# Optimization experiments

Measured on AMD Instinct MI355X. Metric: run time of the kernel, lower is better.

## Reference

```python
import jax, jax.numpy as jnp
import numpy as np

N = 8192
IN_F = 256
OUT_F = 64
ALPHA = 0.3  # LeakyReLU negative slope
NEG_INF = -9e15


def setup_inputs() -> dict:
    key = jax.random.key(0)
    k1, k2, k3, k4 = jax.random.split(key, 4)
    h = jax.random.normal(k1, (N, IN_F), dtype=jnp.float32)
    # sparse-ish binary adjacency with self loops (values are 0/1 floats)
    adj = (jax.random.uniform(k2, (N, N)) < 0.05).astype(jnp.float32)
    adj = jnp.maximum(adj, jnp.eye(N, dtype=jnp.float32))
    # xavier_uniform-style scales (gain=1.414)
    w_lim = 1.414 * np.sqrt(6.0 / (IN_F + OUT_F))
    a_lim = 1.414 * np.sqrt(6.0 / (2 * OUT_F + 1))
    W = jax.random.uniform(k3, (IN_F, OUT_F), minval=-w_lim, maxval=w_lim, dtype=jnp.float32)
    a = jax.random.uniform(k4, (2 * OUT_F, 1), minval=-a_lim, maxval=a_lim, dtype=jnp.float32)
    return {"h": h, "adj": adj, "W": W, "a": a}


def reference(h, adj, W, a):
    # Wh: [N, F]
    Wh = h @ W
    # Additive decomposition of the original concat-attention:
    # e_ij = leakyrelu(a[:F].Wh_i + a[F:].Wh_j)  -- identical math, no NxNx2F tensor
    src = Wh @ a[:OUT_F]      # [N, 1]
    dst = Wh @ a[OUT_F:]      # [N, 1]
    e = jax.nn.leaky_relu(src + dst.T, negative_slope=ALPHA)  # [N, N]
    e = e * adj               # faithful: original multiplies by adj before masking
    att = jnp.where(adj > 0, e, NEG_INF)
    att = jax.nn.softmax(att, axis=1)
    # dropout omitted (eval mode / deterministic reference)
    h_prime = att @ Wh        # [N, F]
    return jax.nn.elu(h_prime)
```

## Files before the change

### kernel.cpp

```cpp
#include <hip/hip_runtime.h>
#include <hip/hip_bf16.h>

#define N_NODES 8192
#define IN_F    256
#define OUT_F   64
#define ALPHA   0.3f
#define MBIAS   20.0f
#define CSPL    8
#define COLS_PER (N_NODES / CSPL)
#define NTILES  (COLS_PER / 64)
#define ROWS    32
#define LDP     72
#define MROW    136

typedef unsigned short u16;
typedef unsigned int   u32;
typedef unsigned long long u64;
typedef __attribute__((ext_vector_type(8))) short bf16x8;
typedef __attribute__((ext_vector_type(4))) float f32x4;

__device__ __forceinline__ float bf2f(u32 u) { return __uint_as_float(u << 16); }
__device__ __forceinline__ u32 f2bfbits(float x) {
    u32 u = __float_as_uint(x);
    return (u + 0x7FFFu + ((u >> 16) & 1u)) >> 16;
}
__device__ __forceinline__ float lrelu(float s) { return s > 0.f ? s : ALPHA * s; }

__device__ __forceinline__ int detect_bf16(const void* adj) {
    return ((((const u32*)adj)[0] & 0xFFFFu) == 0x3F80u) ? 1 : 0;
}

template <bool BF16>
__device__ __forceinline__ float ld(const void* p, size_t idx) {
    if constexpr (BF16) return bf2f(((const u16*)p)[idx]);
    else                return ((const float*)p)[idx];
}

__global__ __launch_bounds__(256) void gat_mask_kernel(
    const void* __restrict__ adj, u64* __restrict__ mask64)
{
    const int lane = threadIdx.x & 63;
    const int wgid = blockIdx.x * 4 + (threadIdx.x >> 6);
    const int NW   = 2048 * 4;
    const int C    = (N_NODES / 256) * N_NODES;

    if (detect_bf16(adj)) {
        const u16* base = (const u16*)adj;
        for (int c = wgid; c < C; c += NW) {
            const u16* p = base + (size_t)c * 256;
            u64 b0 = __ballot(p[lane]       != 0);
            u64 b1 = __ballot(p[64  + lane] != 0);
            u64 b2 = __ballot(p[128 + lane] != 0);
            u64 b3 = __ballot(p[192 + lane] != 0);
            u64 v = (lane == 0) ? b0 : (lane == 1) ? b1 : (lane == 2) ? b2 : b3;
            if (lane < 4) mask64[(size_t)c * 4 + lane] = v;
        }
    } else {
        const float* base = (const float*)adj;
        for (int c = wgid; c < C; c += NW) {
            const float* p = base + (size_t)c * 256;
            u64 b0 = __ballot(p[lane]       != 0.f);
            u64 b1 = __ballot(p[64  + lane] != 0.f);
            u64 b2 = __ballot(p[128 + lane] != 0.f);
            u64 b3 = __ballot(p[192 + lane] != 0.f);
            u64 v = (lane == 0) ? b0 : (lane == 1) ? b1 : (lane == 2) ? b2 : b3;
            if (lane < 4) mask64[(size_t)c * 4 + lane] = v;
        }
    }
}

template <bool BF16>
__device__ __forceinline__ void wh4_impl(
    const void* __restrict__ h, const void* __restrict__ W,
    const void* __restrict__ a, float* __restrict__ src,
    float* __restrict__ dst, int i0, int lane, float* accv)
{
    float acc0 = 0.f, acc1 = 0.f, acc2 = 0.f, acc3 = 0.f;
#pragma unroll 8
    for (int k = 0; k < IN_F; ++k) {
        float wv = ld<BF16>(W, (size_t)k * OUT_F + lane);
        float h0 = ld<BF16>(h, (size_t)(i0 + 0) * IN_F + k);
        float h1 = ld<BF16>(h, (size_t)(i0 + 1) * IN_F + k);
        float h2 = ld<BF16>(h, (size_t)(i0 + 2) * IN_F + k);
        float h3 = ld<BF16>(h, (size_t)(i0 + 3) * IN_F + k);
        acc0 = fmaf(h0, wv, acc0);
        acc1 = fmaf(h1, wv, acc1);
        acc2 = fmaf(h2, wv, acc2);
        acc3 = fmaf(h3, wv, acc3);
    }
    float av = ld<BF16>(a, lane);
    float bv = ld<BF16>(a, OUT_F + lane);
    float accs[4] = {acc0, acc1, acc2, acc3};
#pragma unroll
    for (int r = 0; r < 4; ++r) {
        float ps = accs[r] * av, pd = accs[r] * bv;
#pragma unroll
        for (int off = 32; off > 0; off >>= 1) {
            ps += __shfl_xor(ps, off, 64);
            pd += __shfl_xor(pd, off, 64);
        }
        if (lane == 0) { src[i0 + r] = ps; dst[i0 + r] = pd; }
        accv[r] = accs[r];
    }
}

__global__ __launch_bounds__(256) void gat_wh_kernel(
    const void* __restrict__ h, const void* __restrict__ W,
    const void* __restrict__ a, const void* __restrict__ adj,
    u16* __restrict__ WhT, float* __restrict__ src, float* __restrict__ dst)
{
    __shared__ float accs[16][OUT_F];
    const int tid = threadIdx.x, wave = tid >> 6, lane = tid & 63;
    const int i0 = blockIdx.x * 16 + wave * 4;
    float av[4];
    if (detect_bf16(adj)) wh4_impl<true >(h, W, a, src, dst, i0, lane, av);
    else                  wh4_impl<false>(h, W, a, src, dst, i0, lane, av);
#pragma unroll
    for (int r = 0; r < 4; ++r) accs[wave * 4 + r][lane] = av[r];
    __syncthreads();
    if (tid < OUT_F) {
        u32 w[8];
#pragma unroll
        for (int e = 0; e < 8; ++e) {
            u32 lo = f2bfbits(accs[2 * e][tid]);
            u32 hi = f2bfbits(accs[2 * e + 1][tid]);
            w[e] = lo | (hi << 16);
        }
        u16* dstp = WhT + (size_t)tid * N_NODES + blockIdx.x * 16;
        *(uint4*)dstp       = *(uint4*)&w[0];
        *(uint4*)(dstp + 8) = *(uint4*)&w[4];
    }
}

__global__ __launch_bounds__(256, 4) void gat_attn_kernel(
    const u64* __restrict__ mask64, const u16* __restrict__ WhT,
    const float* __restrict__ src, const float* __restrict__ dst,
    float* __restrict__ O_part, float* __restrict__ l_part)
{
    __shared__ alignas(16) u16 Plds[ROWS * LDP];
    __shared__ alignas(16) u16 Blds[64 * LDP];
    __shared__ alignas(16) unsigned char Mlds[ROWS * MROW];

    const int tid = threadIdx.x, wave = tid >> 6, lane = tid & 63;
    const int r  = tid >> 3, cq = tid & 7;
    const int br = tid >> 2, bq = tid & 3;
    const int i0 = blockIdx.x * ROWS, c0 = blockIdx.y * COLS_PER;

    {
        const unsigned char* mb = (const unsigned char*)mask64;
        uint4 v = *(const uint4*)(mb + (size_t)(i0 + (tid >> 3)) * (N_NODES / 8)
                                     + (c0 >> 3) + (tid & 7) * 16);
        *(uint4*)&Mlds[(tid >> 3) * MROW + (tid & 7) * 16] = v;
    }

    const float srow = src[i0 + r];
    const float m = lrelu(srow + MBIAS);

    const u16*    whtrow = WhT + (size_t)br * N_NODES + c0 + bq * 16;
    const float4* dstp   = (const float4*)(dst + c0 + cq * 8);

    const int mw = wave & 1, nw = wave >> 1;
    const int mrow = lane & 15, kq = (lane >> 4) * 8;

    f32x4 acc[2] = {{0,0,0,0},{0,0,0,0}};
    float lacc = 0.f;

    __syncthreads();

    for (int t = 0; t < NTILES; ++t) {
        uint4 b0 = *(const uint4*)(whtrow + t * 64);
        uint4 b1 = *(const uint4*)(whtrow + t * 64 + 8);
        *(uint4*)&Blds[br * LDP + bq * 16]     = b0;
        *(uint4*)&Blds[br * LDP + bq * 16 + 8] = b1;

        u32 msk = Mlds[r * MROW + t * 8 + cq];
        float4 d0 = dstp[t * 16], d1 = dstp[t * 16 + 1];
        float dv[8] = {d0.x,d0.y,d0.z,d0.w, d1.x,d1.y,d1.z,d1.w};
        u32 po[4];
#pragma unroll
        for (int e = 0; e < 4; ++e) {
            float s0 = lrelu(srow + dv[2 * e]);
            float s1 = lrelu(srow + dv[2 * e + 1]);
            float p0 = (msk & (1u << (2 * e)))     ? __expf(s0 - m) : 0.f;
            float p1 = (msk & (1u << (2 * e + 1))) ? __expf(s1 - m) : 0.f;
            u32 q0 = f2bfbits(p0), q1 = f2bfbits(p1);
            lacc += bf2f(q0) + bf2f(q1);
            po[e] = q0 | (q1 << 16);
        }
        *(uint4*)&Plds[r * LDP + cq * 8] = *(uint4*)&po[0];

        __syncthreads();

#pragma unroll
        for (int ks = 0; ks < 2; ++ks) {
            bf16x8 avf = *(bf16x8*)&Plds[(16 * mw + mrow) * LDP + ks * 32 + kq];
#pragma unroll
            for (int nt2 = 0; nt2 < 2; ++nt2) {
                int nt = nw * 2 + nt2;
                bf16x8 bvf = *(bf16x8*)&Blds[(16 * nt + mrow) * LDP + ks * 32 + kq];
                acc[nt2] = __builtin_amdgcn_mfma_f32_16x16x32_bf16(avf, bvf, acc[nt2], 0, 0, 0);
            }
        }
        __syncthreads();
    }

    lacc += __shfl_xor(lacc, 1, 64);
    lacc += __shfl_xor(lacc, 2, 64);
    lacc += __shfl_xor(lacc, 4, 64);
    if (cq == 0) l_part[blockIdx.y * N_NODES + i0 + r] = lacc;

    float* Ob = O_part + (size_t)blockIdx.y * N_NODES * OUT_F;
#pragma unroll
    for (int nt2 = 0; nt2 < 2; ++nt2) {
        int nt = nw * 2 + nt2;
#pragma unroll
        for (int reg = 0; reg < 4; ++reg) {
            int row = i0 + 16 * mw + (lane >> 4) * 4 + reg;
            int col = 16 * nt + (lane & 15);
            Ob[(size_t)row * OUT_F + col] = acc[nt2][reg];
        }
    }
}

__global__ __launch_bounds__(256) void gat_reduce_kernel(
    const float* __restrict__ O_part, const float* __restrict__ l_part,
    const void* __restrict__ adj, void* __restrict__ out)
{
    int gid = blockIdx.x * 256 + threadIdx.x;
    int i = gid >> 6;
    float O = 0.f, L = 0.f;
#pragma unroll
    for (int c = 0; c < CSPL; ++c) {
        O += O_part[(size_t)c * N_NODES * OUT_F + gid];
        L += l_part[c * N_NODES + i];
    }
    float hp = O / L;
    float o = hp > 0.f ? hp : expm1f(hp);
    if (detect_bf16(adj)) ((u16*)out)[gid] = (u16)f2bfbits(o);
    else                  ((float*)out)[gid] = o;
}

extern "C" void kernel_launch(void* const* d_in, const int* in_sizes, int n_in,
                              void* d_out, int out_size, void* d_ws, size_t ws_size,
                              hipStream_t stream)
{
    const void* h   = d_in[0];
    const void* adj = d_in[1];
    const void* W   = d_in[2];
    const void* a   = d_in[3];

    char* ws = (char*)d_ws;
    u16*   WhT    = (u16*)ws;
    float* src    = (float*)(ws + (1u << 20));
    float* dst    = (float*)(ws + (1u << 20) + 32768);
    u64*   mask64 = (u64*)  (ws + (2u << 20));
    float* O_part = (float*)(ws + (16u << 20));
    float* l_part = (float*)(ws + (32u << 20));

    gat_mask_kernel<<<2048, 256, 0, stream>>>(adj, mask64);
    gat_wh_kernel<<<N_NODES / 16, 256, 0, stream>>>(h, W, a, adj, WhT, src, dst);
    dim3 grid(N_NODES / ROWS, CSPL);
    gat_attn_kernel<<<grid, 256, 0, stream>>>(mask64, WhT, src, dst, O_part, l_part);
    gat_reduce_kernel<<<N_NODES * OUT_F / 256, 256, 0, stream>>>(O_part, l_part, adj, d_out);
}
```

Before: 426.8 us.

## Fuse mask and Wh prep kernels, enlarge attention row tile to 64, prefetch WhT

Merges the adjacency-bitmask kernel and the Wh projection kernel into one launch, splitting the two jobs across block ranges so both run concurrently. The attention kernel now processes 64 rows per block instead of 32, with each wave owning 16 rows across all four output column tiles. This halves how often each WhT tile is reloaded and lets every thread build 16 probabilities per tile. The next WhT tile is also prefetched into registers while the MFMAs run. The costs are more registers, fewer blocks in the grid (1024 rather than 2048), and more LDS per block.

```diff
diff --git a/kernel.cpp b/kernel.cpp
--- a/kernel.cpp
+++ b/kernel.cpp
@@ -9,9 +9,9 @@
 #define CSPL    8
 #define COLS_PER (N_NODES / CSPL)
 #define NTILES  (COLS_PER / 64)
-#define ROWS    32
 #define LDP     72
 #define MROW    136
+#define WH_BLOCKS (N_NODES / 16)
 
 typedef unsigned short u16;
 typedef unsigned int   u32;
@@ -34,39 +34,6 @@
 __device__ __forceinline__ float ld(const void* p, size_t idx) {
     if constexpr (BF16) return bf2f(((const u16*)p)[idx]);
     else                return ((const float*)p)[idx];
-}
-
-__global__ __launch_bounds__(256) void gat_mask_kernel(
-    const void* __restrict__ adj, u64* __restrict__ mask64)
-{
-    const int lane = threadIdx.x & 63;
-    const int wgid = blockIdx.x * 4 + (threadIdx.x >> 6);
-    const int NW   = 2048 * 4;
-    const int C    = (N_NODES / 256) * N_NODES;
-
-    if (detect_bf16(adj)) {
-        const u16* base = (const u16*)adj;
-        for (int c = wgid; c < C; c += NW) {
-            const u16* p = base + (size_t)c * 256;
-            u64 b0 = __ballot(p[lane]       != 0);
-            u64 b1 = __ballot(p[64  + lane] != 0);
-            u64 b2 = __ballot(p[128 + lane] != 0);
-            u64 b3 = __ballot(p[192 + lane] != 0);
-            u64 v = (lane == 0) ? b0 : (lane == 1) ? b1 : (lane == 2) ? b2 : b3;
-            if (lane < 4) mask64[(size_t)c * 4 + lane] = v;
-        }
-    } else {
-        const float* base = (const float*)adj;
-        for (int c = wgid; c < C; c += NW) {
-            const float* p = base + (size_t)c * 256;
-            u64 b0 = __ballot(p[lane]       != 0.f);
-            u64 b1 = __ballot(p[64  + lane] != 0.f);
-            u64 b2 = __ballot(p[128 + lane] != 0.f);
-            u64 b3 = __ballot(p[192 + lane] != 0.f);
-            u64 v = (lane == 0) ? b0 : (lane == 1) ? b1 : (lane == 2) ? b2 : b3;
-            if (lane < 4) mask64[(size_t)c * 4 + lane] = v;
-        }
-    }
 }
 
 template <bool BF16>
@@ -104,31 +71,63 @@
     }
 }
 
-__global__ __launch_bounds__(256) void gat_wh_kernel(
+__global__ __launch_bounds__(256) void gat_prep_kernel(
     const void* __restrict__ h, const void* __restrict__ W,
     const void* __restrict__ a, const void* __restrict__ adj,
-    u16* __restrict__ WhT, float* __restrict__ src, float* __restrict__ dst)
+    u16* __restrict__ WhT, float* __restrict__ src, float* __restrict__ dst,
+    u64* __restrict__ mask64)
 {
     __shared__ float accs[16][OUT_F];
     const int tid = threadIdx.x, wave = tid >> 6, lane = tid & 63;
-    const int i0 = blockIdx.x * 16 + wave * 4;
-    float av[4];
-    if (detect_bf16(adj)) wh4_impl<true >(h, W, a, src, dst, i0, lane, av);
-    else                  wh4_impl<false>(h, W, a, src, dst, i0, lane, av);
-#pragma unroll
-    for (int r = 0; r < 4; ++r) accs[wave * 4 + r][lane] = av[r];
-    __syncthreads();
-    if (tid < OUT_F) {
-        u32 w[8];
-#pragma unroll
-        for (int e = 0; e < 8; ++e) {
-            u32 lo = f2bfbits(accs[2 * e][tid]);
-            u32 hi = f2bfbits(accs[2 * e + 1][tid]);
-            w[e] = lo | (hi << 16);
-        }
-        u16* dstp = WhT + (size_t)tid * N_NODES + blockIdx.x * 16;
-        *(uint4*)dstp       = *(uint4*)&w[0];
-        *(uint4*)(dstp + 8) = *(uint4*)&w[4];
+    const int isbf = detect_bf16(adj);
+
+    if (blockIdx.x < WH_BLOCKS) {
+        const int i0 = blockIdx.x * 16 + wave * 4;
+        float av[4];
+        if (isbf) wh4_impl<true >(h, W, a, src, dst, i0, lane, av);
+        else      wh4_impl<false>(h, W, a, src, dst, i0, lane, av);
+#pragma unroll
+        for (int r = 0; r < 4; ++r) accs[wave * 4 + r][lane] = av[r];
+        __syncthreads();
+        if (tid < OUT_F) {
+            u32 w[8];
+#pragma unroll
+            for (int e = 0; e < 8; ++e) {
+                u32 lo = f2bfbits(accs[2 * e][tid]);
+                u32 hi = f2bfbits(accs[2 * e + 1][tid]);
+                w[e] = lo | (hi << 16);
+            }
+            u16* dstp = WhT + (size_t)tid * N_NODES + blockIdx.x * 16;
+            *(uint4*)dstp       = *(uint4*)&w[0];
+            *(uint4*)(dstp + 8) = *(uint4*)&w[4];
+        }
+    } else {
+        const int wgid = (blockIdx.x - WH_BLOCKS) * 4 + wave;
+        const int NW   = 2048 * 4;
+        const int C    = (N_NODES / 256) * N_NODES;
+        if (isbf) {
+            const u16* base = (const u16*)adj;
+            for (int c = wgid; c < C; c += NW) {
+                const u16* p = base + (size_t)c * 256;
+                u64 b0 = __ballot(p[lane]       != 0);
+                u64 b1 = __ballot(p[64  + lane] != 0);
+                u64 b2 = __ballot(p[128 + lane] != 0);
+                u64 b3 = __ballot(p[192 + lane] != 0);
+                u64 v = (lane == 0) ? b0 : (lane == 1) ? b1 : (lane == 2) ? b2 : b3;
+                if (lane < 4) mask64[(size_t)c * 4 + lane] = v;
+            }
+        } else {
+            const float* base = (const float*)adj;
+            for (int c = wgid; c < C; c += NW) {
+                const float* p = base + (size_t)c * 256;
+                u64 b0 = __ballot(p[lane]       != 0.f);
+                u64 b1 = __ballot(p[64  + lane] != 0.f);
+                u64 b2 = __ballot(p[128 + lane] != 0.f);
+                u64 b3 = __ballot(p[192 + lane] != 0.f);
+                u64 v = (lane == 0) ? b0 : (lane == 1) ? b1 : (lane == 2) ? b2 : b3;
+                if (lane < 4) mask64[(size_t)c * 4 + lane] = v;
+            }
+        }
     }
 }
 
@@ -137,48 +136,50 @@
     const float* __restrict__ src, const float* __restrict__ dst,
     float* __restrict__ O_part, float* __restrict__ l_part)
 {
-    __shared__ alignas(16) u16 Plds[ROWS * LDP];
+    __shared__ alignas(16) u16 Plds[64 * LDP];
     __shared__ alignas(16) u16 Blds[64 * LDP];
-    __shared__ alignas(16) unsigned char Mlds[ROWS * MROW];
+    __shared__ alignas(16) unsigned char Mlds[64 * MROW];
 
     const int tid = threadIdx.x, wave = tid >> 6, lane = tid & 63;
-    const int r  = tid >> 3, cq = tid & 7;
-    const int br = tid >> 2, bq = tid & 3;
-    const int i0 = blockIdx.x * ROWS, c0 = blockIdx.y * COLS_PER;
+    const int r = tid >> 2, cq = tid & 3;
+    const int i0 = blockIdx.x * 64, c0 = blockIdx.y * COLS_PER;
 
     {
-        const unsigned char* mb = (const unsigned char*)mask64;
-        uint4 v = *(const uint4*)(mb + (size_t)(i0 + (tid >> 3)) * (N_NODES / 8)
-                                     + (c0 >> 3) + (tid & 7) * 16);
-        *(uint4*)&Mlds[(tid >> 3) * MROW + (tid & 7) * 16] = v;
+        const unsigned char* g = (const unsigned char*)mask64
+            + (size_t)(i0 + r) * (N_NODES / 8) + (c0 >> 3) + cq * 32;
+        *(uint4*)&Mlds[r * MROW + cq * 32]      = *(const uint4*)g;
+        *(uint4*)&Mlds[r * MROW + cq * 32 + 16] = *(const uint4*)(g + 16);
     }
 
     const float srow = src[i0 + r];
     const float m = lrelu(srow + MBIAS);
 
-    const u16*    whtrow = WhT + (size_t)br * N_NODES + c0 + bq * 16;
-    const float4* dstp   = (const float4*)(dst + c0 + cq * 8);
-
-    const int mw = wave & 1, nw = wave >> 1;
+    const u16*    whtrow = WhT + (size_t)r * N_NODES + c0 + cq * 16;
+    const float4* dstp   = (const float4*)(dst + c0 + cq * 16);
+
     const int mrow = lane & 15, kq = (lane >> 4) * 8;
 
-    f32x4 acc[2] = {{0,0,0,0},{0,0,0,0}};
+    f32x4 acc[4] = {{0,0,0,0},{0,0,0,0},{0,0,0,0},{0,0,0,0}};
     float lacc = 0.f;
 
+    uint4 pb0 = *(const uint4*)(whtrow);
+    uint4 pb1 = *(const uint4*)(whtrow + 8);
+
     __syncthreads();
+    const u16* mrowp = (const u16*)&Mlds[r * MROW];
 
     for (int t = 0; t < NTILES; ++t) {
-        uint4 b0 = *(const uint4*)(whtrow + t * 64);
-        uint4 b1 = *(const uint4*)(whtrow + t * 64 + 8);
-        *(uint4*)&Blds[br * LDP + bq * 16]     = b0;
-        *(uint4*)&Blds[br * LDP + bq * 16 + 8] = b1;
-
-        u32 msk = Mlds[r * MROW + t * 8 + cq];
-        float4 d0 = dstp[t * 16], d1 = dstp[t * 16 + 1];
-        float dv[8] = {d0.x,d0.y,d0.z,d0.w, d1.x,d1.y,d1.z,d1.w};
-        u32 po[4];
-#pragma unroll
-        for (int e = 0; e < 4; ++e) {
+        *(uint4*)&Blds[r * LDP + cq * 16]     = pb0;
+        *(uint4*)&Blds[r * LDP + cq * 16 + 8] = pb1;
+
+        u32 msk = mrowp[t * 4 + cq];
+        float4 d0 = dstp[t * 16],     d1 = dstp[t * 16 + 1];
+        float4 d2 = dstp[t * 16 + 2], d3 = dstp[t * 16 + 3];
+        float dv[16] = {d0.x,d0.y,d0.z,d0.w, d1.x,d1.y,d1.z,d1.w,
+                        d2.x,d2.y,d2.z,d2.w, d3.x,d3.y,d3.z,d3.w};
+        u32 po[8];
+#pragma unroll
+        for (int e = 0; e < 8; ++e) {
             float s0 = lrelu(srow + dv[2 * e]);
             float s1 = lrelu(srow + dv[2 * e + 1]);
             float p0 = (msk & (1u << (2 * e)))     ? __expf(s0 - m) : 0.f;
@@ -187,18 +188,23 @@
             lacc += bf2f(q0) + bf2f(q1);
             po[e] = q0 | (q1 << 16);
         }
-        *(uint4*)&Plds[r * LDP + cq * 8] = *(uint4*)&po[0];
+        *(uint4*)&Plds[r * LDP + cq * 16]     = *(uint4*)&po[0];
+        *(uint4*)&Plds[r * LDP + cq * 16 + 8] = *(uint4*)&po[4];
 
         __syncthreads();
 
+        if (t + 1 < NTILES) {
+            pb0 = *(const uint4*)(whtrow + (t + 1) * 64);
+            pb1 = *(const uint4*)(whtrow + (t + 1) * 64 + 8);
+        }
+
 #pragma unroll
         for (int ks = 0; ks < 2; ++ks) {
-            bf16x8 avf = *(bf16x8*)&Plds[(16 * mw + mrow) * LDP + ks * 32 + kq];
-#pragma unroll
-            for (int nt2 = 0; nt2 < 2; ++nt2) {
-                int nt = nw * 2 + nt2;
+            bf16x8 avf = *(bf16x8*)&Plds[(16 * wave + mrow) * LDP + ks * 32 + kq];
+#pragma unroll
+            for (int nt = 0; nt < 4; ++nt) {
                 bf16x8 bvf = *(bf16x8*)&Blds[(16 * nt + mrow) * LDP + ks * 32 + kq];
-                acc[nt2] = __builtin_amdgcn_mfma_f32_16x16x32_bf16(avf, bvf, acc[nt2], 0, 0, 0);
+                acc[nt] = __builtin_amdgcn_mfma_f32_16x16x32_bf16(avf, bvf, acc[nt], 0, 0, 0);
             }
         }
         __syncthreads();
@@ -206,20 +212,17 @@
 
     lacc += __shfl_xor(lacc, 1, 64);
     lacc += __shfl_xor(lacc, 2, 64);
-    lacc += __shfl_xor(lacc, 4, 64);
     if (cq == 0) l_part[blockIdx.y * N_NODES + i0 + r] = lacc;
 
     float* Ob = O_part + (size_t)blockIdx.y * N_NODES * OUT_F;
 #pragma unroll
-    for (int nt2 = 0; nt2 < 2; ++nt2) {
-        int nt = nw * 2 + nt2;
+    for (int nt = 0; nt < 4; ++nt)
 #pragma unroll
         for (int reg = 0; reg < 4; ++reg) {
-            int row = i0 + 16 * mw + (lane >> 4) * 4 + reg;
+            int row = i0 + 16 * wave + (lane >> 4) * 4 + reg;
             int col = 16 * nt + (lane & 15);
-            Ob[(size_t)row * OUT_F + col] = acc[nt2][reg];
-        }
-    }
+            Ob[(size_t)row * OUT_F + col] = acc[nt][reg];
+        }
 }
 
 __global__ __launch_bounds__(256) void gat_reduce_kernel(
@@ -257,9 +260,8 @@
     float* O_part = (float*)(ws + (16u << 20));
     float* l_part = (float*)(ws + (32u << 20));
 
-    gat_mask_kernel<<<2048, 256, 0, stream>>>(adj, mask64);
-    gat_wh_kernel<<<N_NODES / 16, 256, 0, stream>>>(h, W, a, adj, WhT, src, dst);
-    dim3 grid(N_NODES / ROWS, CSPL);
+    gat_prep_kernel<<<WH_BLOCKS + 2048, 256, 0, stream>>>(h, W, a, adj, WhT, src, dst, mask64);
+    dim3 grid(N_NODES / 64, CSPL);
     gat_attn_kernel<<<grid, 256, 0, stream>>>(mask64, WhT, src, dst, O_part, l_part);
     gat_reduce_kernel<<<N_NODES * OUT_F / 256, 256, 0, stream>>>(O_part, l_part, adj, d_out);
 }
```

Result: no change. 426.8 us (-0.0%).
